# Kernel optimization log

Hardware: AMD Instinct MI355X
Metric: run time of the kernel (lower is better)

Reference implementation:

```python
import math
import jax, jax.numpy as jnp
import numpy as np

DIM = 4096
N_HEADS = 32
N_KV_HEADS = 8
HEAD_DIM = DIM // N_HEADS        # 128
N_REP = N_HEADS // N_KV_HEADS    # 4
BSZ = 1
SEQ = 2048
ROPE_THETA = 500000.0


def setup_inputs() -> dict:
    key = jax.random.key(0)
    ks = jax.random.split(key, 5)
    scale = 1.0 / math.sqrt(DIM)
    x = jax.random.normal(ks[0], (BSZ, SEQ, DIM), dtype=jnp.float32)
    wq = jax.random.normal(ks[1], (N_HEADS * HEAD_DIM, DIM), dtype=jnp.float32) * scale
    wk = jax.random.normal(ks[2], (N_KV_HEADS * HEAD_DIM, DIM), dtype=jnp.float32) * scale
    wv = jax.random.normal(ks[3], (N_KV_HEADS * HEAD_DIM, DIM), dtype=jnp.float32) * scale
    wo = jax.random.normal(ks[4], (N_HEADS * HEAD_DIM, DIM), dtype=jnp.float32).T * scale
    wo = jnp.asarray(wo)  # [DIM, N_HEADS*HEAD_DIM] like nn.Linear(in=heads*hd, out=dim).weight
    # RoPE tables: freqs_cis[t, j] = exp(i * t * theta^{-2j/head_dim}), j in [0, head_dim/2)
    inv_freq = 1.0 / (ROPE_THETA ** (np.arange(0, HEAD_DIM, 2, dtype=np.float32) / HEAD_DIM))
    t = np.arange(SEQ, dtype=np.float32)
    ang = np.outer(t, inv_freq)  # [SEQ, HEAD_DIM//2]
    freqs_cos = jnp.asarray(np.cos(ang), dtype=jnp.float32)
    freqs_sin = jnp.asarray(np.sin(ang), dtype=jnp.float32)
    # additive causal mask [SEQ, SEQ]
    mask = jnp.where(jnp.tril(jnp.ones((SEQ, SEQ), dtype=bool)), 0.0, -1e9).astype(jnp.float32)
    return {"x": x, "wq": wq, "wk": wk, "wv": wv, "wo": wo,
            "freqs_cos": freqs_cos, "freqs_sin": freqs_sin, "mask": mask}


def _apply_rope(xh, cos, sin):
    # xh: [b, s, h, head_dim]; cos/sin: [s, head_dim//2]
    b, s, h, d = xh.shape
    xr = xh.reshape(b, s, h, d // 2, 2)
    x0, x1 = xr[..., 0], xr[..., 1]
    c = cos[None, :, None, :]
    sn = sin[None, :, None, :]
    o0 = x0 * c - x1 * sn
    o1 = x0 * sn + x1 * c
    return jnp.stack([o0, o1], axis=-1).reshape(b, s, h, d)


def reference(x, wq, wk, wv, wo, freqs_cos, freqs_sin, mask):
    bsz, seqlen, _ = x.shape
    xq = (x @ wq.T).reshape(bsz, seqlen, N_HEADS, HEAD_DIM)
    xk = (x @ wk.T).reshape(bsz, seqlen, N_KV_HEADS, HEAD_DIM)
    xv = (x @ wv.T).reshape(bsz, seqlen, N_KV_HEADS, HEAD_DIM)
    xq = _apply_rope(xq, freqs_cos, freqs_sin)
    xk = _apply_rope(xk, freqs_cos, freqs_sin)
    # repeat_kv (GQA expansion)
    keys = jnp.repeat(xk, N_REP, axis=2)    # [b, s, N_HEADS, hd]
    values = jnp.repeat(xv, N_REP, axis=2)
    scores = jnp.einsum('bqhd,bkhd->bhqk', xq, keys) / math.sqrt(HEAD_DIM)
    scores = scores + mask[None, None, :, :]
    scores = jax.nn.softmax(scores.astype(jnp.float32), axis=-1).astype(xq.dtype)
    out = jnp.einsum('bhqk,bkhd->bqhd', scores, values)
    out = out.reshape(bsz, seqlen, N_HEADS * HEAD_DIM)
    return out @ wo.T
```

## Files before the change

### kernel.cpp

```cpp
#include <hip/hip_runtime.h>
#include <math.h>
#include <stdint.h>
#include <stddef.h>


typedef __attribute__((ext_vector_type(8))) short bf16x8;
typedef __attribute__((ext_vector_type(4))) short bf16x4;
typedef __attribute__((ext_vector_type(4))) float f32x4;
typedef unsigned short u16;

#define NEG_BIG (-1.0e9f)
#define MFMA32(a, b, c) __builtin_amdgcn_mfma_f32_16x16x32_bf16(a, b, c, 0, 0, 0)
#define SFENCE() __builtin_amdgcn_sched_barrier(0)

__device__ __forceinline__ float bf2f(u16 b) {
    return __uint_as_float(((unsigned int)b) << 16);
}
__device__ __forceinline__ u16 f2bf(float f) {
    unsigned int u = __float_as_uint(f);
    u += 0x7fff + ((u >> 16) & 1);
    return (u16)(u >> 16);
}
__device__ __forceinline__ void gld_lds16(short* lds, const u16* g) {
    __builtin_amdgcn_global_load_lds(
        (const __attribute__((address_space(1))) void*)g,
        (__attribute__((address_space(3))) void*)lds, 16, 0, 0);
}

__global__ __launch_bounds__(256) void cvt_all(
    const float* __restrict__ x, const float* __restrict__ wq,
    const float* __restrict__ wk, const float* __restrict__ wv,
    const float* __restrict__ wo,
    u16* __restrict__ xb, u16* __restrict__ wqb, u16* __restrict__ wkb,
    u16* __restrict__ wvb, u16* __restrict__ wob) {
    const int b = blockIdx.x;
    const float* s; u16* d; int off;
    if (b < 4096)       { s = x;  d = xb;  off = b; }
    else if (b < 12288) { s = wq; d = wqb; off = b - 4096; }
    else if (b < 14336) { s = wk; d = wkb; off = b - 12288; }
    else if (b < 16384) { s = wv; d = wvb; off = b - 14336; }
    else                { s = wo; d = wob; off = b - 16384; }
    const int i = off * 2048 + threadIdx.x * 8;
    float4 a, c;
    __builtin_memcpy(&a, s + i, 16);
    __builtin_memcpy(&c, s + i + 4, 16);
    bf16x8 o;
    o[0] = (short)f2bf(a.x); o[1] = (short)f2bf(a.y);
    o[2] = (short)f2bf(a.z); o[3] = (short)f2bf(a.w);
    o[4] = (short)f2bf(c.x); o[5] = (short)f2bf(c.y);
    o[6] = (short)f2bf(c.z); o[7] = (short)f2bf(c.w);
    __builtin_memcpy(d + i, &o, 16);
}


#define G8_STGA(bf_, ks_, kt_)                                               \
    {                                                                        \
        _Pragma("unroll") for (int r_ = 0; r_ < RA; ++r_)                    \
            gld_lds16(Ad + (bf_) * AT + (ks_) * AH + r_ * 4096,              \
                      Ag + gK * r_ + (size_t)(kt_) * 64 + (ks_) * 32);       \
    }
#define G8_STGB(bf_, ks_, kt_)                                               \
    {                                                                        \
        _Pragma("unroll") for (int r_ = 0; r_ < RB; ++r_)                    \
            gld_lds16(Bd + (bf_) * BT + (ks_) * BH + r_ * 4096,              \
                      Bg + gK * r_ + (size_t)(kt_) * 64 + (ks_) * 32);       \
    }
#define G8_PHASE(bf_, ks_, mh_, RDB_, STAGE_, WAIT_)                         \
    {                                                                        \
        if (RDB_) {                                                          \
            _Pragma("unroll") for (int n_ = 0; n_ < 4; ++n_)                 \
                __builtin_memcpy(&bfr[n_], Bs + (bf_) * BT + (ks_) * BH +    \
                                               bbase + n_ * 512, 16);        \
        }                                                                    \
        _Pragma("unroll") for (int i_ = 0; i_ < 4; ++i_)                     \
            __builtin_memcpy(&af[i_], S + (bf_) * AT + (ks_) * AH + abase +  \
                                          ((mh_) * 64 + i_ * 16) * 32, 16);  \
        STAGE_;                                                              \
        SFENCE();                                                            \
        __builtin_amdgcn_s_barrier();                                        \
        asm volatile("s_waitcnt lgkmcnt(0)" ::: "memory");                   \
        SFENCE();                                                            \
        __builtin_amdgcn_s_setprio(1);                                       \
        _Pragma("unroll") for (int i_ = 0; i_ < 4; ++i_)                     \
            _Pragma("unroll") for (int n_ = 0; n_ < 4; ++n_)                 \
                acc[(mh_) * 4 + i_][n_] =                                    \
                    MFMA32(af[i_], bfr[n_], acc[(mh_) * 4 + i_][n_]);        \
        __builtin_amdgcn_s_setprio(0);                                       \
        SFENCE();                                                            \
        WAIT_;                                                               \
        __builtin_amdgcn_s_barrier();                                        \
    }

template <int BM, int BN, int MH, int OUT>
__device__ __forceinline__ void gemm8p(const u16* __restrict__ A,
                                       const u16* __restrict__ B,
                                       void* __restrict__ C,
                                       int mb, int nb, int N, int K,
                                       short* __restrict__ S) {
    constexpr int AT = BM * 64, BT = BN * 64;
    constexpr int AH = BM * 32, BH = BN * 32;
    constexpr int RA = BM / 128, RB = BN / 128;
    short* const Bs = S + 2 * AT;

    const int t = threadIdx.x;
    const int lane = t & 63, l15 = lane & 15, quad = lane >> 4;
    const int wid = t >> 6, wr = wid >> 2, wc = wid & 3;

    const int srow = t >> 2;
    const int cs = (t & 3) ^ ((t >> 3) & 3);
    const u16* const Ag = A + (size_t)(mb * BM + srow) * K + cs * 8;
    const u16* const Bg = B + (size_t)(nb * BN + srow) * K + cs * 8;
    short* const Ad = S + t * 8;
    short* const Bd = Bs + t * 8;
    const size_t gK = (size_t)128 * K;

    const int swz = (quad ^ ((l15 >> 1) & 3)) * 8;
    const int abase = (wr * (BM / 2) + l15) * 32 + swz;
    const int bbase = (wc * 64 + l15) * 32 + swz;

    f32x4 acc[MH * 4][4] = {};
    bf16x8 af[4], bfr[4];

    G8_STGA(0, 0, 0); G8_STGB(0, 0, 0);
    G8_STGA(0, 1, 0); G8_STGB(0, 1, 0);
    G8_STGA(1, 0, 1); G8_STGB(1, 0, 1);
    if constexpr (MH == 2) {
        asm volatile("s_waitcnt vmcnt(4)" ::: "memory");
    } else {
        asm volatile("s_waitcnt vmcnt(6)" ::: "memory");
    }
    __builtin_amdgcn_s_barrier();

    const int nIt = K >> 7;
    if constexpr (MH == 2) {
        for (int it = 0; it < nIt; ++it) {
            const int k0 = 2 * it, k1 = k0 + 1;
            const bool nl = (it < nIt - 1);
            G8_PHASE(0, 0, 0, true,  G8_STGA(1, 1, k1), );
            G8_PHASE(0, 0, 1, false, G8_STGB(1, 1, k1), );
            G8_PHASE(0, 1, 0, true,  if (nl) G8_STGA(0, 0, k0 + 2), );
            G8_PHASE(0, 1, 1, false, if (nl) G8_STGB(0, 0, k0 + 2),
                     if (nl) { asm volatile("s_waitcnt vmcnt(4)" ::: "memory"); }
                     else    { asm volatile("s_waitcnt vmcnt(0)" ::: "memory"); });
            G8_PHASE(1, 0, 0, true,  if (nl) G8_STGA(0, 1, k0 + 2), );
            G8_PHASE(1, 0, 1, false, if (nl) G8_STGB(0, 1, k0 + 2), );
            G8_PHASE(1, 1, 0, true,  if (nl) G8_STGA(1, 0, k1 + 2), );
            G8_PHASE(1, 1, 1, false, if (nl) G8_STGB(1, 0, k1 + 2),
                     if (nl) { asm volatile("s_waitcnt vmcnt(4)" ::: "memory"); });
        }
    } else {
        for (int it = 0; it < nIt - 1; ++it) {
            const int k0 = 2 * it, k1 = k0 + 1;
            G8_PHASE(0, 0, 0, true, { G8_STGA(1, 1, k1); G8_STGB(1, 1, k1); },
                     asm volatile("s_waitcnt vmcnt(6)" ::: "memory"));
            G8_PHASE(0, 1, 0, true, { G8_STGA(0, 0, k0 + 2); G8_STGB(0, 0, k0 + 2); },
                     asm volatile("s_waitcnt vmcnt(6)" ::: "memory"));
            G8_PHASE(1, 0, 0, true, { G8_STGA(0, 1, k0 + 2); G8_STGB(0, 1, k0 + 2); },
                     asm volatile("s_waitcnt vmcnt(6)" ::: "memory"));
            G8_PHASE(1, 1, 0, true, { G8_STGA(1, 0, k1 + 2); G8_STGB(1, 0, k1 + 2); },
                     asm volatile("s_waitcnt vmcnt(6)" ::: "memory"));
        }
        {
            const int k1 = (K >> 6) - 1;
            G8_PHASE(0, 0, 0, true, { G8_STGA(1, 1, k1); G8_STGB(1, 1, k1); },
                     asm volatile("s_waitcnt vmcnt(6)" ::: "memory"));
            G8_PHASE(0, 1, 0, true, ,
                     asm volatile("s_waitcnt vmcnt(3)" ::: "memory"));
            G8_PHASE(1, 0, 0, true, ,
                     asm volatile("s_waitcnt vmcnt(0)" ::: "memory"));
            G8_PHASE(1, 1, 0, true, , );
        }
    }

#pragma unroll
    for (int i8 = 0; i8 < MH * 4; ++i8) {
        const int rowb = mb * BM + wr * (BM / 2) + (i8 >> 2) * 64 +
                         (i8 & 3) * 16 + quad * 4;
#pragma unroll
        for (int j = 0; j < 4; ++j) {
            const int col = nb * BN + wc * 64 + j * 16 + l15;
            if (OUT == 2) {
                bf16x4 v;
#pragma unroll
                for (int r = 0; r < 4; ++r) v[r] = (short)f2bf(acc[i8][j][r]);
                __builtin_memcpy((u16*)C + (size_t)col * 2048 + rowb, &v, 8);
            } else if (OUT == 1) {
#pragma unroll
                for (int r = 0; r < 4; ++r)
                    ((float*)C)[(size_t)(rowb + r) * N + col] = acc[i8][j][r];
            } else {
#pragma unroll
                for (int r = 0; r < 4; ++r)
                    ((u16*)C)[(size_t)(rowb + r) * N + col] =
                        f2bf(acc[i8][j][r]);
            }
        }
    }
}

__global__ __launch_bounds__(512, 2) void qkv_proj8(
    const u16* __restrict__ x,
    const u16* __restrict__ wq, const u16* __restrict__ wk,
    const u16* __restrict__ wv,
    u16* __restrict__ Q, u16* __restrict__ Kc, u16* __restrict__ Vt) {
    __shared__ __align__(16) short S[65536];
    const int lid = blockIdx.x;
    const int swzb = (lid & 7) * 24 + (lid >> 3);
    const int mb = swzb & 7, y = swzb >> 3;
    if (y < 16)
        gemm8p<256, 256, 2, 0>(x, wq, Q, mb, y, 4096, 4096, S);
    else if (y < 20)
        gemm8p<256, 256, 2, 0>(x, wk, Kc, mb, y - 16, 1024, 4096, S);
    else
        gemm8p<256, 256, 2, 2>(x, wv, Vt, mb, y - 20, 1024, 4096, S);
}

__global__ __launch_bounds__(512, 2) void oproj8(
    const u16* __restrict__ A, const u16* __restrict__ wo,
    float* __restrict__ out) {
    __shared__ __align__(16) short S[49152];
    const int lid = blockIdx.x;
    const int logical = (lid & 7) * 32 + (lid >> 3);
    const int mb = logical & 15, nb = logical >> 4;
    gemm8p<128, 256, 1, 1>(A, wo, out, mb, nb, 4096, 4096, S);
}

__global__ __launch_bounds__(256) void rope_all(
    u16* __restrict__ Q, u16* __restrict__ Kc,
    const float* __restrict__ cosb, const float* __restrict__ sinb) {
    const int idx = blockIdx.x * blockDim.x + threadIdx.x;
    const int i = idx & 63;
    const int hh = (idx >> 6) % 40;
    const int s = (idx >> 6) / 40;
    u16* p;
    if (hh < 32)
        p = Q + (size_t)s * 4096 + hh * 128 + 2 * i;
    else
        p = Kc + (size_t)s * 1024 + (hh - 32) * 128 + 2 * i;
    const float x0 = bf2f(p[0]), x1 = bf2f(p[1]);
    const float c = cosb[s * 64 + i], sn = sinb[s * 64 + i];
    p[0] = f2bf(x0 * c - x1 * sn);
    p[1] = f2bf(x0 * sn + x1 * c);
}

__device__ __forceinline__ int kswz(int row, int cs) {
    int f = (row & 3) | ((row & 8) >> 1);
    return row * 128 + ((cs ^ f) << 3);
}

template <bool MASKED>
__device__ __forceinline__ void fa_step_lds(
    const short* __restrict__ Kl, const short* __restrict__ Vl,
    int kb, int q0, int l15, int quad,
    const int (&koff)[8], const int (&voff)[8],
    const bf16x8 (&qf)[4], f32x4 (&o)[8], float& m, float& l) {
    const float scale = 0.08838834764831845f;

    bf16x8 kf[8];
#pragma unroll
    for (int i = 0; i < 8; ++i) __builtin_memcpy(&kf[i], Kl + koff[i], 16);
    f32x4 s0 = {0, 0, 0, 0}, s1 = {0, 0, 0, 0};
#pragma unroll
    for (int c = 0; c < 4; ++c) {
        s0 = MFMA32(kf[c], qf[c], s0);
        s1 = MFMA32(kf[4 + c], qf[c], s1);
    }

    bf16x8 vf[8];
#pragma unroll
    for (int n = 0; n < 8; ++n) __builtin_memcpy(&vf[n], Vl + voff[n], 16);

    float sv0[4], sv1[4];
    const int q = q0 + l15;
#pragma unroll
    for (int r = 0; r < 4; ++r) {
        sv0[r] = s0[r] * scale;
        sv1[r] = s1[r] * scale;
        if (MASKED) {
            if (kb + 8 * quad + r > q) sv0[r] = NEG_BIG;
            if (kb + 8 * quad + 4 + r > q) sv1[r] = NEG_BIG;
        }
    }

    float mx = fmaxf(fmaxf(fmaxf(sv0[0], sv0[1]), fmaxf(sv0[2], sv0[3])),
                     fmaxf(fmaxf(sv1[0], sv1[1]), fmaxf(sv1[2], sv1[3])));
    mx = fmaxf(mx, __shfl_xor(mx, 16));
    mx = fmaxf(mx, __shfl_xor(mx, 32));

    float alpha = 1.0f;
    if (!__all(mx <= m + 8.0f)) {
        float mnew = fmaxf(m, mx);
        alpha = __expf(m - mnew);
        float aO[4];
#pragma unroll
        for (int r = 0; r < 4; ++r) aO[r] = __shfl(alpha, quad * 20 + r);
#pragma unroll
        for (int n = 0; n < 8; ++n)
#pragma unroll
            for (int r = 0; r < 4; ++r) o[n][r] *= aO[r];
        m = mnew;
    }

    float p0[4], p1[4], sum = 0.f;
#pragma unroll
    for (int r = 0; r < 4; ++r) {
        p0[r] = __expf(sv0[r] - m);
        p1[r] = __expf(sv1[r] - m);
        sum += p0[r] + p1[r];
    }
    sum += __shfl_xor(sum, 16);
    sum += __shfl_xor(sum, 32);
    l = l * alpha + sum;

    bf16x8 pa;
#pragma unroll
    for (int r = 0; r < 4; ++r) {
        pa[r] = (short)f2bf(p0[r]);
        pa[4 + r] = (short)f2bf(p1[r]);
    }

#pragma unroll
    for (int n = 0; n < 8; ++n) o[n] = MFMA32(pa, vf[n], o[n]);
}

__device__ __forceinline__ void fa_task(
    const u16* __restrict__ Q, const u16* __restrict__ Kc,
    const u16* __restrict__ Vt, u16* __restrict__ O,
    short* __restrict__ Kl0, short* __restrict__ Vl0,
    int q0, int nbt, int h, int kvh, int t) {
    const int lane = t & 63;
    const int l15 = lane & 15, quad = lane >> 4;

    bf16x8 qf[4];
    const u16* qp = Q + (size_t)(q0 + l15) * 4096 + h * 128 + quad * 8;
#pragma unroll
    for (int c = 0; c < 4; ++c) __builtin_memcpy(&qf[c], qp + c * 32, 16);

    const u16* ksrc[2]; short* kdst[2];
    const u16* vsrc[2]; short* vdst[2];
#pragma unroll
    for (int r = 0; r < 2; ++r) {
        int row = (t >> 4) + 16 * r;
        int slot = t & 15;
        int f = (row & 3) | ((row & 8) >> 1);
        int cks = slot ^ f;
        ksrc[r] = Kc + (size_t)row * 1024 + kvh * 128 + cks * 8;
        kdst[r] = Kl0 + (t + 256 * r) * 8;
        int rowv = (t >> 2) + 64 * r;
        int csv = (t & 3) ^ ((t >> 3) & 3);
        vsrc[r] = Vt + (size_t)(kvh * 128 + rowv) * 2048 + csv * 8;
        vdst[r] = Vl0 + (t + 256 * r) * 8;
    }

    const int rk0 = 8 * (l15 >> 2) + (l15 & 3);
    int koff[8], voff[8];
#pragma unroll
    for (int c = 0; c < 4; ++c) {
        koff[c] = kswz(rk0, quad + c * 4);
        koff[4 + c] = kswz(rk0 + 4, quad + c * 4);
    }
    const int vswz = (quad ^ ((l15 >> 1) & 3)) * 8;
#pragma unroll
    for (int n = 0; n < 8; ++n) voff[n] = (n * 16 + l15) * 32 + vswz;

    f32x4 o[8] = {};
    float m = NEG_BIG, l = 0.f;
    const int my_nb = (q0 + 47) / 32;

    {
        gld_lds16(kdst[0], ksrc[0]);
        gld_lds16(kdst[1], ksrc[1]);
        gld_lds16(vdst[0], vsrc[0]);
        gld_lds16(vdst[1], vsrc[1]);
    }
    __syncthreads();

    for (int ib = 0; ib < nbt; ++ib) {
        if (ib + 1 < nbt) {
            int kb = (ib + 1) * 32;
            int bo = ((ib + 1) & 1) * 4096;
            gld_lds16(kdst[0] + bo, ksrc[0] + (size_t)kb * 1024);
            gld_lds16(kdst[1] + bo, ksrc[1] + (size_t)kb * 1024);
            gld_lds16(vdst[0] + bo, vsrc[0] + kb);
            gld_lds16(vdst[1] + bo, vsrc[1] + kb);
        }
        if (ib < my_nb) {
            const short* Kl = Kl0 + (ib & 1) * 4096;
            const short* Vl = Vl0 + (ib & 1) * 4096;
            if (ib == my_nb - 1)
                fa_step_lds<true>(Kl, Vl, ib * 32, q0, l15, quad, koff, voff,
                                  qf, o, m, l);
            else
                fa_step_lds<false>(Kl, Vl, ib * 32, q0, l15, quad, koff, voff,
                                   qf, o, m, l);
        }
        __syncthreads();
    }

    float inv[4];
#pragma unroll
    for (int r = 0; r < 4; ++r) inv[r] = 1.f / __shfl(l, quad * 20 + r);
#pragma unroll
    for (int n = 0; n < 8; ++n)
#pragma unroll
        for (int r = 0; r < 4; ++r) {
            int row = q0 + quad * 4 + r;
            O[(size_t)row * 4096 + h * 128 + n * 16 + l15] =
                f2bf(o[n][r] * inv[r]);
        }
}

__global__ __launch_bounds__(256) void flash_attn(
    const u16* __restrict__ Q, const u16* __restrict__ Kc,
    const u16* __restrict__ Vt, u16* __restrict__ O) {
    __shared__ __align__(16) short Kl[2 * 32 * 128];
    __shared__ __align__(16) short Vl[2 * 128 * 32];
    const int pp = blockIdx.x;
    const int h = blockIdx.y;
    const int kvh = h >> 2;
    const int t = threadIdx.x, wave = t >> 6;
    fa_task(Q, Kc, Vt, O, Kl, Vl, pp * 64 + wave * 16, 2 * pp + 2, h, kvh, t);
    const int tb = 31 - pp;
    fa_task(Q, Kc, Vt, O, Kl, Vl, tb * 64 + (3 - wave) * 16, 2 * tb + 2, h,
            kvh, t);
}

extern "C" void kernel_launch(void* const* d_in, const int* in_sizes, int n_in,
                              void* d_out, int out_size, void* d_ws,
                              size_t ws_size, hipStream_t stream) {
    const float* x  = (const float*)d_in[0];
    const float* wq = (const float*)d_in[1];
    const float* wk = (const float*)d_in[2];
    const float* wv = (const float*)d_in[3];
    const float* wo = (const float*)d_in[4];
    const float* fc = (const float*)d_in[5];
    const float* fs = (const float*)d_in[6];
    float* out = (float*)d_out;

    const int NX = 2048 * 4096;
    const int NQW = 4096 * 4096;
    const int NKW = 1024 * 4096;
    const int NKV = 2048 * 1024;

    u16* Q   = (u16*)d_ws;
    u16* Kc  = Q   + NX;
    u16* Vt  = Kc  + NKV;
    u16* Ao  = Vt  + NKV;
    u16* xb  = Ao  + NX;
    u16* wqb = xb  + NX;
    u16* wkb = wqb + NQW;
    u16* wvb = wkb + NKW;
    u16* wob = wvb + NKW;

    cvt_all<<<24576, 256, 0, stream>>>(x, wq, wk, wv, wo,
                                       xb, wqb, wkb, wvb, wob);
    qkv_proj8<<<192, 512, 0, stream>>>(xb, wqb, wkb, wvb, Q, Kc, Vt);
    rope_all<<<20480, 256, 0, stream>>>(Q, Kc, fc, fs);
    flash_attn<<<dim3(16, 32), 256, 0, stream>>>(Q, Kc, Vt, Ao);
    oproj8<<<256, 512, 0, stream>>>(Ao, wob, out);
}
```

Before: 487.2 us.

## Double-buffer LDS fragment registers to overlap reads with MFMA in projection GEMMs

Rewrites the QKV and output projection GEMM main loops to use two register banks for A/B fragments. Each phase now issues the LDS reads for the next phase while MFMAs run on the current bank. This removes the per-phase lgkmcnt(0) wait and one of the two barriers per phase, hiding LDS latency behind matrix math. In exchange it uses more VGPRs and needs a hand-tuned vmcnt schedule, which risks register pressure and subtle ordering hazards.

```diff
diff --git a/kernel.cpp b/kernel.cpp
--- a/kernel.cpp
+++ b/kernel.cpp
@@ -12,6 +12,8 @@
 #define NEG_BIG (-1.0e9f)
 #define MFMA32(a, b, c) __builtin_amdgcn_mfma_f32_16x16x32_bf16(a, b, c, 0, 0, 0)
 #define SFENCE() __builtin_amdgcn_sched_barrier(0)
+#define BAR() __builtin_amdgcn_s_barrier()
+#define VMW(n_) asm volatile("s_waitcnt vmcnt(" #n_ ")" ::: "memory")
 
 __device__ __forceinline__ float bf2f(u16 b) {
     return __uint_as_float(((unsigned int)b) << 16);
@@ -53,141 +55,102 @@
 }
 
 
-#define G8_STGA(bf_, ks_, kt_)                                               \
+#define QSTGA(bf_, ks_, kt_)                                                 \
+    { _Pragma("unroll") for (int r_ = 0; r_ < 2; ++r_)                       \
+        gld_lds16(Ad + (bf_) * 16384 + (ks_) * 8192 + r_ * 4096,             \
+                  Ag + gK * r_ + (size_t)(kt_) * 64 + (ks_) * 32); }
+#define QSTGB(bf_, ks_, kt_)                                                 \
+    { _Pragma("unroll") for (int r_ = 0; r_ < 2; ++r_)                       \
+        gld_lds16(Bd + (bf_) * 16384 + (ks_) * 8192 + r_ * 4096,             \
+                  Bg + gK * r_ + (size_t)(kt_) * 64 + (ks_) * 32); }
+#define QRDA(bank_, bf_, ks_, mh_)                                           \
+    { _Pragma("unroll") for (int i_ = 0; i_ < 4; ++i_)                       \
+        __builtin_memcpy(&bank_[i_], S + (bf_) * 16384 + (ks_) * 8192 +      \
+                         abase + ((mh_) * 64 + i_ * 16) * 32, 16); }
+#define QRDB(bank_, bf_, ks_)                                                \
+    { _Pragma("unroll") for (int n_ = 0; n_ < 4; ++n_)                       \
+        __builtin_memcpy(&bank_[n_], Bs + (bf_) * 16384 + (ks_) * 8192 +     \
+                         bbase + n_ * 512, 16); }
+#define QMM(afb_, bfb_, mh_)                                                 \
     {                                                                        \
-        _Pragma("unroll") for (int r_ = 0; r_ < RA; ++r_)                    \
-            gld_lds16(Ad + (bf_) * AT + (ks_) * AH + r_ * 4096,              \
-                      Ag + gK * r_ + (size_t)(kt_) * 64 + (ks_) * 32);       \
-    }
-#define G8_STGB(bf_, ks_, kt_)                                               \
-    {                                                                        \
-        _Pragma("unroll") for (int r_ = 0; r_ < RB; ++r_)                    \
-            gld_lds16(Bd + (bf_) * BT + (ks_) * BH + r_ * 4096,              \
-                      Bg + gK * r_ + (size_t)(kt_) * 64 + (ks_) * 32);       \
-    }
-#define G8_PHASE(bf_, ks_, mh_, RDB_, STAGE_, WAIT_)                         \
-    {                                                                        \
-        if (RDB_) {                                                          \
-            _Pragma("unroll") for (int n_ = 0; n_ < 4; ++n_)                 \
-                __builtin_memcpy(&bfr[n_], Bs + (bf_) * BT + (ks_) * BH +    \
-                                               bbase + n_ * 512, 16);        \
-        }                                                                    \
-        _Pragma("unroll") for (int i_ = 0; i_ < 4; ++i_)                     \
-            __builtin_memcpy(&af[i_], S + (bf_) * AT + (ks_) * AH + abase +  \
-                                          ((mh_) * 64 + i_ * 16) * 32, 16);  \
-        STAGE_;                                                              \
-        SFENCE();                                                            \
-        __builtin_amdgcn_s_barrier();                                        \
-        asm volatile("s_waitcnt lgkmcnt(0)" ::: "memory");                   \
-        SFENCE();                                                            \
         __builtin_amdgcn_s_setprio(1);                                       \
         _Pragma("unroll") for (int i_ = 0; i_ < 4; ++i_)                     \
             _Pragma("unroll") for (int n_ = 0; n_ < 4; ++n_)                 \
                 acc[(mh_) * 4 + i_][n_] =                                    \
-                    MFMA32(af[i_], bfr[n_], acc[(mh_) * 4 + i_][n_]);        \
+                    MFMA32(afb_[i_], bfb_[n_], acc[(mh_) * 4 + i_][n_]);     \
         __builtin_amdgcn_s_setprio(0);                                       \
-        SFENCE();                                                            \
-        WAIT_;                                                               \
-        __builtin_amdgcn_s_barrier();                                        \
-    }
-
-template <int BM, int BN, int MH, int OUT>
-__device__ __forceinline__ void gemm8p(const u16* __restrict__ A,
+    }
+
+template <int OUT>
+__device__ __forceinline__ void gemm_q(const u16* __restrict__ A,
                                        const u16* __restrict__ B,
                                        void* __restrict__ C,
                                        int mb, int nb, int N, int K,
                                        short* __restrict__ S) {
-    constexpr int AT = BM * 64, BT = BN * 64;
-    constexpr int AH = BM * 32, BH = BN * 32;
-    constexpr int RA = BM / 128, RB = BN / 128;
-    short* const Bs = S + 2 * AT;
-
+    short* const Bs = S + 32768;
     const int t = threadIdx.x;
     const int lane = t & 63, l15 = lane & 15, quad = lane >> 4;
     const int wid = t >> 6, wr = wid >> 2, wc = wid & 3;
 
     const int srow = t >> 2;
     const int cs = (t & 3) ^ ((t >> 3) & 3);
-    const u16* const Ag = A + (size_t)(mb * BM + srow) * K + cs * 8;
-    const u16* const Bg = B + (size_t)(nb * BN + srow) * K + cs * 8;
+    const u16* const Ag = A + (size_t)(mb * 256 + srow) * K + cs * 8;
+    const u16* const Bg = B + (size_t)(nb * 256 + srow) * K + cs * 8;
     short* const Ad = S + t * 8;
     short* const Bd = Bs + t * 8;
     const size_t gK = (size_t)128 * K;
 
     const int swz = (quad ^ ((l15 >> 1) & 3)) * 8;
-    const int abase = (wr * (BM / 2) + l15) * 32 + swz;
+    const int abase = (wr * 128 + l15) * 32 + swz;
     const int bbase = (wc * 64 + l15) * 32 + swz;
 
-    f32x4 acc[MH * 4][4] = {};
-    bf16x8 af[4], bfr[4];
-
-    G8_STGA(0, 0, 0); G8_STGB(0, 0, 0);
-    G8_STGA(0, 1, 0); G8_STGB(0, 1, 0);
-    G8_STGA(1, 0, 1); G8_STGB(1, 0, 1);
-    if constexpr (MH == 2) {
-        asm volatile("s_waitcnt vmcnt(4)" ::: "memory");
-    } else {
-        asm volatile("s_waitcnt vmcnt(6)" ::: "memory");
-    }
-    __builtin_amdgcn_s_barrier();
+    f32x4 acc[8][4] = {};
+    bf16x8 af0[4], af1[4], bf0[4], bf1[4];
+
+    QSTGA(0, 0, 0); QSTGB(0, 0, 0);
+    QSTGA(0, 1, 0); QSTGB(0, 1, 0);
+    QSTGA(1, 0, 1); QSTGB(1, 0, 1);
+    VMW(8);
+    BAR();
+    QRDA(af0, 0, 0, 0); QRDB(bf0, 0, 0);
+    SFENCE();
 
     const int nIt = K >> 7;
-    if constexpr (MH == 2) {
-        for (int it = 0; it < nIt; ++it) {
-            const int k0 = 2 * it, k1 = k0 + 1;
-            const bool nl = (it < nIt - 1);
-            G8_PHASE(0, 0, 0, true,  G8_STGA(1, 1, k1), );
-            G8_PHASE(0, 0, 1, false, G8_STGB(1, 1, k1), );
-            G8_PHASE(0, 1, 0, true,  if (nl) G8_STGA(0, 0, k0 + 2), );
-            G8_PHASE(0, 1, 1, false, if (nl) G8_STGB(0, 0, k0 + 2),
-                     if (nl) { asm volatile("s_waitcnt vmcnt(4)" ::: "memory"); }
-                     else    { asm volatile("s_waitcnt vmcnt(0)" ::: "memory"); });
-            G8_PHASE(1, 0, 0, true,  if (nl) G8_STGA(0, 1, k0 + 2), );
-            G8_PHASE(1, 0, 1, false, if (nl) G8_STGB(0, 1, k0 + 2), );
-            G8_PHASE(1, 1, 0, true,  if (nl) G8_STGA(1, 0, k1 + 2), );
-            G8_PHASE(1, 1, 1, false, if (nl) G8_STGB(1, 0, k1 + 2),
-                     if (nl) { asm volatile("s_waitcnt vmcnt(4)" ::: "memory"); });
-        }
-    } else {
-        for (int it = 0; it < nIt - 1; ++it) {
-            const int k0 = 2 * it, k1 = k0 + 1;
-            G8_PHASE(0, 0, 0, true, { G8_STGA(1, 1, k1); G8_STGB(1, 1, k1); },
-                     asm volatile("s_waitcnt vmcnt(6)" ::: "memory"));
-            G8_PHASE(0, 1, 0, true, { G8_STGA(0, 0, k0 + 2); G8_STGB(0, 0, k0 + 2); },
-                     asm volatile("s_waitcnt vmcnt(6)" ::: "memory"));
-            G8_PHASE(1, 0, 0, true, { G8_STGA(0, 1, k0 + 2); G8_STGB(0, 1, k0 + 2); },
-                     asm volatile("s_waitcnt vmcnt(6)" ::: "memory"));
-            G8_PHASE(1, 1, 0, true, { G8_STGA(1, 0, k1 + 2); G8_STGB(1, 0, k1 + 2); },
-                     asm volatile("s_waitcnt vmcnt(6)" ::: "memory"));
-        }
-        {
-            const int k1 = (K >> 6) - 1;
-            G8_PHASE(0, 0, 0, true, { G8_STGA(1, 1, k1); G8_STGB(1, 1, k1); },
-                     asm volatile("s_waitcnt vmcnt(6)" ::: "memory"));
-            G8_PHASE(0, 1, 0, true, ,
-                     asm volatile("s_waitcnt vmcnt(3)" ::: "memory"));
-            G8_PHASE(1, 0, 0, true, ,
-                     asm volatile("s_waitcnt vmcnt(0)" ::: "memory"));
-            G8_PHASE(1, 1, 0, true, , );
-        }
-    }
-
-#pragma unroll
-    for (int i8 = 0; i8 < MH * 4; ++i8) {
-        const int rowb = mb * BM + wr * (BM / 2) + (i8 >> 2) * 64 +
+    for (int it = 0; it < nIt - 1; ++it) {
+        const int k1 = 2 * it + 1, kn0 = 2 * it + 2, kn1 = 2 * it + 3;
+        QSTGA(1, 1, k1);  QRDA(af1, 0, 0, 1);                    QMM(af0, bf0, 0); SFENCE(); VMW(6); BAR();
+        QSTGB(1, 1, k1);  QRDA(af0, 0, 1, 0); QRDB(bf1, 0, 1);   QMM(af1, bf0, 1); SFENCE();         BAR();
+        QSTGA(0, 0, kn0); QRDA(af1, 0, 1, 1);                    QMM(af0, bf1, 0); SFENCE(); VMW(6); BAR();
+        QSTGB(0, 0, kn0); QRDA(af0, 1, 0, 0); QRDB(bf0, 1, 0);   QMM(af1, bf1, 1); SFENCE();         BAR();
+        QSTGA(0, 1, kn0); QRDA(af1, 1, 0, 1);                    QMM(af0, bf0, 0); SFENCE(); VMW(6); BAR();
+        QSTGB(0, 1, kn0); QRDA(af0, 1, 1, 0); QRDB(bf1, 1, 1);   QMM(af1, bf0, 1); SFENCE();         BAR();
+        QSTGA(1, 0, kn1); QRDA(af1, 1, 1, 1);                    QMM(af0, bf1, 0); SFENCE(); VMW(6); BAR();
+        QSTGB(1, 0, kn1); QRDA(af0, 0, 0, 0); QRDB(bf0, 0, 0);   QMM(af1, bf1, 1); SFENCE();         BAR();
+    }
+    {
+        const int k1 = 2 * nIt - 1;
+        QSTGA(1, 1, k1);  QRDA(af1, 0, 0, 1);                    QMM(af0, bf0, 0); SFENCE(); VMW(6); BAR();
+        QSTGB(1, 1, k1);  QRDA(af0, 0, 1, 0); QRDB(bf1, 0, 1);   QMM(af1, bf0, 1); SFENCE();         BAR();
+        QRDA(af1, 0, 1, 1);                                      QMM(af0, bf1, 0); SFENCE(); VMW(4); BAR();
+        QRDA(af0, 1, 0, 0); QRDB(bf0, 1, 0);                     QMM(af1, bf1, 1); SFENCE();         BAR();
+        QRDA(af1, 1, 0, 1);                                      QMM(af0, bf0, 0); SFENCE(); VMW(0); BAR();
+        QRDA(af0, 1, 1, 0); QRDB(bf1, 1, 1);                     QMM(af1, bf0, 1); SFENCE();         BAR();
+        QRDA(af1, 1, 1, 1);                                      QMM(af0, bf1, 0); SFENCE();         BAR();
+        QMM(af1, bf1, 1);
+    }
+
+#pragma unroll
+    for (int i8 = 0; i8 < 8; ++i8) {
+        const int rowb = mb * 256 + wr * 128 + (i8 >> 2) * 64 +
                          (i8 & 3) * 16 + quad * 4;
 #pragma unroll
         for (int j = 0; j < 4; ++j) {
-            const int col = nb * BN + wc * 64 + j * 16 + l15;
+            const int col = nb * 256 + wc * 64 + j * 16 + l15;
             if (OUT == 2) {
                 bf16x4 v;
 #pragma unroll
                 for (int r = 0; r < 4; ++r) v[r] = (short)f2bf(acc[i8][j][r]);
                 __builtin_memcpy((u16*)C + (size_t)col * 2048 + rowb, &v, 8);
-            } else if (OUT == 1) {
-#pragma unroll
-                for (int r = 0; r < 4; ++r)
-                    ((float*)C)[(size_t)(rowb + r) * N + col] = acc[i8][j][r];
             } else {
 #pragma unroll
                 for (int r = 0; r < 4; ++r)
@@ -208,21 +171,100 @@
     const int swzb = (lid & 7) * 24 + (lid >> 3);
     const int mb = swzb & 7, y = swzb >> 3;
     if (y < 16)
-        gemm8p<256, 256, 2, 0>(x, wq, Q, mb, y, 4096, 4096, S);
+        gemm_q<0>(x, wq, Q, mb, y, 4096, 4096, S);
     else if (y < 20)
-        gemm8p<256, 256, 2, 0>(x, wk, Kc, mb, y - 16, 1024, 4096, S);
+        gemm_q<0>(x, wk, Kc, mb, y - 16, 1024, 4096, S);
     else
-        gemm8p<256, 256, 2, 2>(x, wv, Vt, mb, y - 20, 1024, 4096, S);
-}
+        gemm_q<2>(x, wv, Vt, mb, y - 20, 1024, 4096, S);
+}
+
+
+#define OSTG(bf_, ks_, kt_)                                                  \
+    {                                                                        \
+        gld_lds16(Ad + (bf_) * 8192 + (ks_) * 4096,                          \
+                  Ag + (size_t)(kt_) * 64 + (ks_) * 32);                     \
+        _Pragma("unroll") for (int r_ = 0; r_ < 2; ++r_)                     \
+            gld_lds16(Bd + (bf_) * 16384 + (ks_) * 8192 + r_ * 4096,         \
+                      Bg + gK * r_ + (size_t)(kt_) * 64 + (ks_) * 32);       \
+    }
+#define ORDA(bank_, bf_, ks_)                                                \
+    { _Pragma("unroll") for (int i_ = 0; i_ < 4; ++i_)                       \
+        __builtin_memcpy(&bank_[i_], S + (bf_) * 8192 + (ks_) * 4096 +       \
+                         abase + i_ * 512, 16); }
+#define ORDB(bank_, bf_, ks_)                                                \
+    { _Pragma("unroll") for (int n_ = 0; n_ < 4; ++n_)                       \
+        __builtin_memcpy(&bank_[n_], Bs + (bf_) * 16384 + (ks_) * 8192 +     \
+                         bbase + n_ * 512, 16); }
+#define OMM(afb_, bfb_)                                                      \
+    {                                                                        \
+        __builtin_amdgcn_s_setprio(1);                                       \
+        _Pragma("unroll") for (int i_ = 0; i_ < 4; ++i_)                     \
+            _Pragma("unroll") for (int n_ = 0; n_ < 4; ++n_)                 \
+                acc[i_][n_] = MFMA32(afb_[i_], bfb_[n_], acc[i_][n_]);       \
+        __builtin_amdgcn_s_setprio(0);                                       \
+    }
 
 __global__ __launch_bounds__(512, 2) void oproj8(
     const u16* __restrict__ A, const u16* __restrict__ wo,
     float* __restrict__ out) {
     __shared__ __align__(16) short S[49152];
+    short* const Bs = S + 16384;
     const int lid = blockIdx.x;
     const int logical = (lid & 7) * 32 + (lid >> 3);
     const int mb = logical & 15, nb = logical >> 4;
-    gemm8p<128, 256, 1, 1>(A, wo, out, mb, nb, 4096, 4096, S);
+
+    const int t = threadIdx.x;
+    const int lane = t & 63, l15 = lane & 15, quad = lane >> 4;
+    const int wid = t >> 6, wr = wid >> 2, wc = wid & 3;
+
+    const int srow = t >> 2;
+    const int cs = (t & 3) ^ ((t >> 3) & 3);
+    const u16* const Ag = A + (size_t)(mb * 128 + srow) * 4096 + cs * 8;
+    const u16* const Bg = wo + (size_t)(nb * 256 + srow) * 4096 + cs * 8;
+    short* const Ad = S + t * 8;
+    short* const Bd = Bs + t * 8;
+    const size_t gK = (size_t)128 * 4096;
+
+    const int swz = (quad ^ ((l15 >> 1) & 3)) * 8;
+    const int abase = (wr * 64 + l15) * 32 + swz;
+    const int bbase = (wc * 64 + l15) * 32 + swz;
+
+    f32x4 acc[4][4] = {};
+    bf16x8 af0[4], af1[4], bf0[4], bf1[4];
+
+    OSTG(0, 0, 0); OSTG(0, 1, 0); OSTG(1, 0, 1);
+    VMW(3);
+    BAR();
+    ORDA(af0, 0, 0); ORDB(bf0, 0, 0);
+    SFENCE();
+
+    const int nIt = 32;
+    for (int it = 0; it < nIt - 1; ++it) {
+        const int k1 = 2 * it + 1, kn0 = 2 * it + 2, kn1 = 2 * it + 3;
+        OSTG(1, 1, k1);  ORDA(af1, 0, 1); ORDB(bf1, 0, 1); OMM(af0, bf0); SFENCE(); VMW(3); BAR();
+        OSTG(0, 0, kn0); ORDA(af0, 1, 0); ORDB(bf0, 1, 0); OMM(af1, bf1); SFENCE(); VMW(3); BAR();
+        OSTG(0, 1, kn0); ORDA(af1, 1, 1); ORDB(bf1, 1, 1); OMM(af0, bf0); SFENCE(); VMW(3); BAR();
+        OSTG(1, 0, kn1); ORDA(af0, 0, 0); ORDB(bf0, 0, 0); OMM(af1, bf1); SFENCE(); VMW(3); BAR();
+    }
+    {
+        const int k1 = 2 * nIt - 1;
+        OSTG(1, 1, k1);  ORDA(af1, 0, 1); ORDB(bf1, 0, 1); OMM(af0, bf0); SFENCE(); VMW(3); BAR();
+        ORDA(af0, 1, 0); ORDB(bf0, 1, 0);                  OMM(af1, bf1); SFENCE(); VMW(0); BAR();
+        ORDA(af1, 1, 1); ORDB(bf1, 1, 1);                  OMM(af0, bf0); SFENCE();         BAR();
+        OMM(af1, bf1);
+    }
+
+#pragma unroll
+    for (int i = 0; i < 4; ++i) {
+        const int rowb = mb * 128 + wr * 64 + i * 16 + quad * 4;
+#pragma unroll
+        for (int j = 0; j < 4; ++j) {
+            const int col = nb * 256 + wc * 64 + j * 16 + l15;
+#pragma unroll
+            for (int r = 0; r < 4; ++r)
+                out[(size_t)(rowb + r) * 4096 + col] = acc[i][j][r];
+        }
+    }
 }
 
 __global__ __launch_bounds__(256) void rope_all(
```

New measurement: 512.6 us. +5.2%, slower.
